# Performance work log

Measured on AMD Instinct MI355X. Metric: run time of the kernel, lower is better.

## Reference

```python
import jax, jax.numpy as jnp
import numpy as np
import math

IN_DIM = 512
OUT_DIM = 512
K = 64
N_BANDS = 3
TOTAL_K = K * N_BANDS
SCALE = 0.1
XAVIER_SCALE = math.sqrt(2.0 / (IN_DIM + OUT_DIM))


def setup_inputs() -> dict:
    key = jax.random.key(0)
    k_x, k_om, k_phi, k_a, k_ab = jax.random.split(key, 5)
    x = jax.random.normal(k_x, (8, 1024, IN_DIM), dtype=jnp.float32)
    # omega: per-band frequency scaling 1 + 3*band
    band_scales = jnp.repeat(1.0 + 3.0 * jnp.arange(N_BANDS, dtype=jnp.float32), K)  # (TOTAL_K,)
    omega = jax.random.normal(k_om, (TOTAL_K, 3), dtype=jnp.float32) * band_scales[:, None]
    phi = jax.random.normal(k_phi, (TOTAL_K,), dtype=jnp.float32) * math.pi
    n_coeff = 2 * TOTAL_K
    decay = 1.0 + jnp.arange(n_coeff, dtype=jnp.float32)
    alpha = jax.random.normal(k_a, (n_coeff,), dtype=jnp.float32) * 0.01 / decay
    alpha_bias = jax.random.normal(k_ab, (n_coeff,), dtype=jnp.float32) * 0.001
    return {"x": x, "omega": omega, "phi": phi, "alpha": alpha,
            "alpha_bias": alpha_bias, "layer_idx": 2, "num_layers": 6}


def _positions(layer_idx, num_layers):
    l_val = (layer_idx + 1.0) / (num_layers + 1.0)
    i_idx = (jnp.arange(IN_DIM, dtype=jnp.float32) + 1.0) / (IN_DIM + 1.0)
    j_idx = (jnp.arange(OUT_DIM, dtype=jnp.float32) + 1.0) / (OUT_DIM + 1.0)
    ii, jj = jnp.meshgrid(i_idx, j_idx, indexing='ij')
    ll = jnp.full_like(ii, l_val)
    pw = jnp.stack([ii, jj, ll], axis=-1).reshape(-1, 3)  # (IN*OUT, 3)
    pb = jnp.stack([jnp.zeros_like(j_idx), j_idx, jnp.full_like(j_idx, l_val)], axis=-1)  # (OUT, 3)
    return pw, pb


def reference(x, omega, phi, alpha, alpha_bias, layer_idx, num_layers):
    pw, pb = _positions(float(layer_idx), float(num_layers))
    # weight synthesis: tiny-K matmul -> sin/cos features -> reduce with alpha
    args = pw @ omega.T + phi                       # (IN*OUT, TOTAL_K)
    features = jnp.concatenate([jnp.sin(args), jnp.cos(args)], axis=1)  # (IN*OUT, 2K)
    W = (features @ alpha * SCALE).reshape(IN_DIM, OUT_DIM) * (XAVIER_SCALE / SCALE)
    # bias synthesis
    bargs = pb @ omega.T + phi                      # (OUT, TOTAL_K)
    bfeat = jnp.concatenate([jnp.sin(bargs), jnp.cos(bargs)], axis=1)
    b = bfeat @ alpha_bias * SCALE * 0.2            # (OUT,)
    return x @ W + b
```

## Files before the change

### kernel.cpp

```cpp
#include <hip/hip_runtime.h>
#include <hip/hip_bf16.h>
#include <math.h>

#define IN_DIM   512
#define OUT_DIM  512
#define NK       192
#define KF       384
#define XAVIER   0.04419417382415922f
#define BIAS_SCALE 0.02f

typedef __attribute__((ext_vector_type(8))) short bf16x8;
typedef __attribute__((ext_vector_type(4))) float f32x4;
typedef unsigned short u16;
typedef unsigned int   u32;
typedef unsigned long long u64;

__device__ inline u16 f2bf(float f) {
    __hip_bfloat16 h = __float2bfloat16(f);
    return *reinterpret_cast<u16*>(&h);
}
__device__ inline u32 pack2bf(float lo, float hi) {
    return (u32)f2bf(lo) | ((u32)f2bf(hi) << 16);
}
__device__ inline void gload_lds16(const void* g, void* l) {
    __builtin_amdgcn_global_load_lds(
        (const __attribute__((address_space(1))) void*)g,
        (__attribute__((address_space(3))) void*)l, 16, 0, 0);
}
__device__ inline void fsincos(float x, float& s, float& c) {
    float t = x * 0.15915494309189535f;
    t -= floorf(t);
    s = __builtin_amdgcn_sinf(t);
    c = __builtin_amdgcn_cosf(t);
}

__global__ __launch_bounds__(512) void synth_fused(
    const float* __restrict__ omega, const float* __restrict__ phi,
    const float* __restrict__ alpha, const float* __restrict__ alpha_bias,
    const int* __restrict__ layer_idx, const int* __restrict__ num_layers,
    u16* __restrict__ Wt, float* __restrict__ bias)
{
    const int b   = blockIdx.x;
    const int tid = threadIdx.x;
    const float l = ((float)layer_idx[0] + 1.0f) / ((float)num_layers[0] + 1.0f);

    __shared__ u16 sV[32 * KF];
    __shared__ u16 sU[32 * KF];
    __shared__ float bsc[4];

    const int bi = b & 15, bj = b >> 4;
    const int i0 = bi * 32, j0 = bj * 32;

    #pragma unroll 4
    for (int q = 0; q < 12; ++q) {
        const int e  = q * 512 + tid;
        const int rl = e / NK;
        const int k  = e - rl * NK;
        const int swz  = (rl & 7) << 4;
        const int base = rl * (KF * 2);
        const float om0 = omega[3*k], om1 = omega[3*k+1], om2 = omega[3*k+2];
        const float ph  = phi[k];
        {
            const float ii = (i0 + rl + 1.0f) * (1.0f / (IN_DIM + 1.0f));
            float s, c; fsincos(fmaf(ii, om0, fmaf(l, om2, ph)), s, c);
            *(u16*)((char*)sU + base + (((2*k)      ) ^ swz)) = f2bf(s);
            *(u16*)((char*)sU + base + (((2*k) + 384) ^ swz)) = f2bf(c);
        }
        {
            const float jj = (j0 + rl + 1.0f) * (1.0f / (OUT_DIM + 1.0f));
            float sv, cv; fsincos(jj * om1, sv, cv);
            const float as = alpha[k], ac = alpha[NK + k];
            *(u16*)((char*)sV + base + (((2*k)      ) ^ swz)) = f2bf((as*cv - ac*sv) * XAVIER);
            *(u16*)((char*)sV + base + (((2*k) + 384) ^ swz)) = f2bf((ac*cv + as*sv) * XAVIER);
        }
    }

    if (tid >= 256) {
        const int t2 = tid - 256;
        const int g  = t2 >> 7;
        const int k0 = t2 & 127;
        const int j  = 2*b + g;
        const float jj = (j + 1.0f) * (1.0f / (OUT_DIM + 1.0f));
        float bp = 0.0f;
        {
            float s, c;
            fsincos(fmaf(jj, omega[3*k0+1], fmaf(l, omega[3*k0+2], phi[k0])), s, c);
            bp = fmaf(alpha_bias[k0], s, fmaf(alpha_bias[NK + k0], c, bp));
        }
        if (k0 < 64) {
            const int k = k0 + 128;
            float s, c;
            fsincos(fmaf(jj, omega[3*k+1], fmaf(l, omega[3*k+2], phi[k])), s, c);
            bp = fmaf(alpha_bias[k], s, fmaf(alpha_bias[NK + k], c, bp));
        }
        #pragma unroll
        for (int off = 32; off > 0; off >>= 1)
            bp += __shfl_down(bp, off);
        if ((tid & 63) == 0) bsc[t2 >> 6] = bp;
    }
    __syncthreads();

    if (tid < 256) {
        const int wave = tid >> 6, lane = tid & 63;
        const int wr = wave >> 1, wc = wave & 1;
        f32x4 acc = {};
        #pragma unroll
        for (int kk = 0; kk < KF / 32; ++kk) {
            const int kb = kk * 64 + (lane >> 4) * 16;
            const int ra = wr*16 + (lane & 15);
            const int rb = wc*16 + (lane & 15);
            bf16x8 a = *reinterpret_cast<const bf16x8*>(
                (const char*)sV + ra*768 + (kb ^ ((ra & 7) << 4)));
            bf16x8 bb = *reinterpret_cast<const bf16x8*>(
                (const char*)sU + rb*768 + (kb ^ ((rb & 7) << 4)));
            acc = __builtin_amdgcn_mfma_f32_16x16x32_bf16(a, bb, acc, 0, 0, 0);
        }
        const int row = j0 + wr*16 + (lane >> 4) * 4;
        const int col = i0 + wc*16 + (lane & 15);
        #pragma unroll
        for (int r = 0; r < 4; ++r)
            Wt[(size_t)(row + r) * IN_DIM + col] = f2bf(acc[r]);
    }
    if (tid == 256) bias[2*b    ] = (bsc[0] + bsc[1]) * BIAS_SCALE;
    if (tid == 257) bias[2*b + 1] = (bsc[2] + bsc[3]) * BIAS_SCALE;
}

__global__ __launch_bounds__(512) void main_gemm(
    const float* __restrict__ X, const u16* __restrict__ Wt,
    const float* __restrict__ bias, float* __restrict__ out, int M)
{
    __shared__ u16 sA[2][32 * 64];
    __shared__ u16 sB[2][512 * 64];

    const int tid  = threadIdx.x;
    const int w    = tid >> 6, lane = tid & 63;
    const int brow = blockIdx.x * 32;

    f32x4 acc[2][4] = {};

    const int bsrc  = ((lane & 7) * 16) ^ ((lane >> 3) << 4);
    const int bjrow = lane >> 3;
    const int arow = tid >> 4;
    const int akq  = tid & 15;
    const int adst = arow * 128 + (((akq * 8)) ^ ((arow & 7) << 4));
    const size_t xoff = (size_t)(brow + arow) * IN_DIM + akq * 4;

    auto stageB = [&](int buf, int k0) {
        #pragma unroll
        for (int c = 0; c < 8; ++c) {
            const int ci = w * 8 + c;
            const int j  = ci * 8 + bjrow;
            gload_lds16((const char*)Wt + (size_t)j * (IN_DIM * 2) + k0 * 2 + bsrc,
                        (char*)&sB[buf][0] + ci * 1024);
        }
    };
    auto loadA = [&](int k0) -> f32x4 {
        return *reinterpret_cast<const f32x4*>(&X[xoff + k0]);
    };
    auto writeA = [&](int buf, f32x4 v) {
        u64 p = (u64)pack2bf(v.x, v.y) | ((u64)pack2bf(v.z, v.w) << 32);
        *reinterpret_cast<u64*>((char*)&sA[buf][0] + adst) = p;
    };
    auto compute = [&](int buf) {
        #pragma unroll
        for (int kk = 0; kk < 2; ++kk) {
            const int kb = kk * 64 + (lane >> 4) * 16;
            bf16x8 a[2], bb[4];
            #pragma unroll
            for (int m = 0; m < 2; ++m) {
                const int r = m*16 + (lane & 15);
                a[m] = *reinterpret_cast<const bf16x8*>(
                    (const char*)&sA[buf][0] + r*128 + (kb ^ ((r & 7) << 4)));
            }
            #pragma unroll
            for (int n = 0; n < 4; ++n) {
                const int j = w*64 + n*16 + (lane & 15);
                bb[n] = *reinterpret_cast<const bf16x8*>(
                    (const char*)&sB[buf][0] + j*128 + (kb ^ ((j & 7) << 4)));
            }
            #pragma unroll
            for (int m = 0; m < 2; ++m)
                #pragma unroll
                for (int n = 0; n < 4; ++n)
                    acc[m][n] = __builtin_amdgcn_mfma_f32_16x16x32_bf16(
                        a[m], bb[n], acc[m][n], 0, 0, 0);
        }
    };

    #define VMW(n)  asm volatile("s_waitcnt vmcnt(" #n ")" ::: "memory")
    #define LGKM0   asm volatile("s_waitcnt lgkmcnt(0)" ::: "memory")
    #define BARRIER do { __builtin_amdgcn_s_barrier(); \
                         asm volatile("" ::: "memory"); } while (0)

    {
        f32x4 av = loadA(0);
        stageB(0, 0);
        VMW(8);
        writeA(0, av);
        av = loadA(64);
        stageB(1, 64);
        VMW(8);
        writeA(1, av);
        LGKM0;
        BARRIER;
    }

    #pragma unroll
    for (int t = 0; t < 8; ++t) {
        compute(t & 1);
        BARRIER;
        if (t < 6) {
            f32x4 av = loadA((t + 2) * 64);
            stageB(t & 1, (t + 2) * 64);
            VMW(8);
            writeA(t & 1, av);
        } else if (t == 6) {
            VMW(0);
        }
        LGKM0;
        BARRIER;
    }

    #undef VMW
    #undef LGKM0
    #undef BARRIER

    #pragma unroll
    for (int n = 0; n < 4; ++n) {
        const int col = w*64 + n*16 + (lane & 15);
        const float bv = bias[col];
        #pragma unroll
        for (int m = 0; m < 2; ++m) {
            const int row0 = brow + m*16 + (lane >> 4) * 4;
            #pragma unroll
            for (int r = 0; r < 4; ++r)
                out[(size_t)(row0 + r) * OUT_DIM + col] = acc[m][n][r] + bv;
        }
    }
}

extern "C" void kernel_launch(void* const* d_in, const int* in_sizes, int n_in,
                              void* d_out, int out_size, void* d_ws, size_t ws_size,
                              hipStream_t stream) {
    const float* x          = (const float*)d_in[0];
    const float* omega      = (const float*)d_in[1];
    const float* phi        = (const float*)d_in[2];
    const float* alpha      = (const float*)d_in[3];
    const float* alpha_bias = (const float*)d_in[4];
    const int*   layer_idx  = (const int*)d_in[5];
    const int*   num_layers = (const int*)d_in[6];
    float* out = (float*)d_out;

    const int M = in_sizes[0] / IN_DIM;

    u16*   Wt   = (u16*)d_ws;
    float* bias = (float*)((char*)d_ws + 512 * 1024);

    synth_fused<<<256, 512, 0, stream>>>(omega, phi, alpha, alpha_bias,
                                         layer_idx, num_layers, Wt, bias);
    main_gemm<<<M / 32, 512, 0, stream>>>(x, Wt, bias, out, M);
}
```

Baseline: 24.14 us.

## Fuse weight synthesis and main GEMM into one kernel with grid barrier

Merges the synthesis kernel and the GEMM kernel into a single launch of M/32=256 blocks. Each block first synthesizes its weight tile and bias slice, then prefetches its first two X slices and waits on a global atomic counter until every block has finished, after which it runs the GEMM. The aim is to remove the second kernel launch and the gap between kernels, and to overlap the X loads with synthesis. In exchange it adds a memset launch and a spin-wait grid barrier. That barrier is only safe while all 256 blocks are co-resident, which the 136KB of shared memory per block makes dependent on CU count and occupancy.

Result: slower. 41.38 us (+71.4%).

```diff
diff --git a/kernel.cpp b/kernel.cpp
--- a/kernel.cpp
+++ b/kernel.cpp
@@ -34,110 +34,105 @@
     c = __builtin_amdgcn_cosf(t);
 }
 
-__global__ __launch_bounds__(512) void synth_fused(
+__global__ __launch_bounds__(512) void fourier_fused(
+    const float* __restrict__ X,
     const float* __restrict__ omega, const float* __restrict__ phi,
     const float* __restrict__ alpha, const float* __restrict__ alpha_bias,
     const int* __restrict__ layer_idx, const int* __restrict__ num_layers,
-    u16* __restrict__ Wt, float* __restrict__ bias)
+    u16* __restrict__ Wt, float* __restrict__ bias,
+    u32* __restrict__ ctr, float* __restrict__ out, int M)
 {
+    __shared__ __align__(16) char smem[136 * 1024];
+    char* const sA  = smem;
+    char* const sB  = smem + 8 * 1024;
+    char*  const sU  = smem + 72 * 1024;
+    char*  const sV  = smem + 96 * 1024;
+    float* const bsc = (float*)(smem + 120 * 1024);
+
     const int b   = blockIdx.x;
     const int tid = threadIdx.x;
     const float l = ((float)layer_idx[0] + 1.0f) / ((float)num_layers[0] + 1.0f);
 
-    __shared__ u16 sV[32 * KF];
-    __shared__ u16 sU[32 * KF];
-    __shared__ float bsc[4];
-
-    const int bi = b & 15, bj = b >> 4;
-    const int i0 = bi * 32, j0 = bj * 32;
-
-    #pragma unroll 4
-    for (int q = 0; q < 12; ++q) {
-        const int e  = q * 512 + tid;
-        const int rl = e / NK;
-        const int k  = e - rl * NK;
-        const int swz  = (rl & 7) << 4;
-        const int base = rl * (KF * 2);
-        const float om0 = omega[3*k], om1 = omega[3*k+1], om2 = omega[3*k+2];
-        const float ph  = phi[k];
-        {
-            const float ii = (i0 + rl + 1.0f) * (1.0f / (IN_DIM + 1.0f));
-            float s, c; fsincos(fmaf(ii, om0, fmaf(l, om2, ph)), s, c);
-            *(u16*)((char*)sU + base + (((2*k)      ) ^ swz)) = f2bf(s);
-            *(u16*)((char*)sU + base + (((2*k) + 384) ^ swz)) = f2bf(c);
-        }
-        {
-            const float jj = (j0 + rl + 1.0f) * (1.0f / (OUT_DIM + 1.0f));
-            float sv, cv; fsincos(jj * om1, sv, cv);
-            const float as = alpha[k], ac = alpha[NK + k];
-            *(u16*)((char*)sV + base + (((2*k)      ) ^ swz)) = f2bf((as*cv - ac*sv) * XAVIER);
-            *(u16*)((char*)sV + base + (((2*k) + 384) ^ swz)) = f2bf((ac*cv + as*sv) * XAVIER);
-        }
-    }
-
-    if (tid >= 256) {
-        const int t2 = tid - 256;
-        const int g  = t2 >> 7;
-        const int k0 = t2 & 127;
-        const int j  = 2*b + g;
-        const float jj = (j + 1.0f) * (1.0f / (OUT_DIM + 1.0f));
-        float bp = 0.0f;
-        {
-            float s, c;
-            fsincos(fmaf(jj, omega[3*k0+1], fmaf(l, omega[3*k0+2], phi[k0])), s, c);
-            bp = fmaf(alpha_bias[k0], s, fmaf(alpha_bias[NK + k0], c, bp));
-        }
-        if (k0 < 64) {
-            const int k = k0 + 128;
-            float s, c;
-            fsincos(fmaf(jj, omega[3*k+1], fmaf(l, omega[3*k+2], phi[k])), s, c);
-            bp = fmaf(alpha_bias[k], s, fmaf(alpha_bias[NK + k], c, bp));
-        }
-        #pragma unroll
-        for (int off = 32; off > 0; off >>= 1)
-            bp += __shfl_down(bp, off);
-        if ((tid & 63) == 0) bsc[t2 >> 6] = bp;
-    }
-    __syncthreads();
-
-    if (tid < 256) {
-        const int wave = tid >> 6, lane = tid & 63;
-        const int wr = wave >> 1, wc = wave & 1;
-        f32x4 acc = {};
-        #pragma unroll
-        for (int kk = 0; kk < KF / 32; ++kk) {
-            const int kb = kk * 64 + (lane >> 4) * 16;
-            const int ra = wr*16 + (lane & 15);
-            const int rb = wc*16 + (lane & 15);
-            bf16x8 a = *reinterpret_cast<const bf16x8*>(
-                (const char*)sV + ra*768 + (kb ^ ((ra & 7) << 4)));
-            bf16x8 bb = *reinterpret_cast<const bf16x8*>(
-                (const char*)sU + rb*768 + (kb ^ ((rb & 7) << 4)));
-            acc = __builtin_amdgcn_mfma_f32_16x16x32_bf16(a, bb, acc, 0, 0, 0);
-        }
-        const int row = j0 + wr*16 + (lane >> 4) * 4;
-        const int col = i0 + wc*16 + (lane & 15);
-        #pragma unroll
-        for (int r = 0; r < 4; ++r)
-            Wt[(size_t)(row + r) * IN_DIM + col] = f2bf(acc[r]);
-    }
-    if (tid == 256) bias[2*b    ] = (bsc[0] + bsc[1]) * BIAS_SCALE;
-    if (tid == 257) bias[2*b + 1] = (bsc[2] + bsc[3]) * BIAS_SCALE;
-}
-
-__global__ __launch_bounds__(512) void main_gemm(
-    const float* __restrict__ X, const u16* __restrict__ Wt,
-    const float* __restrict__ bias, float* __restrict__ out, int M)
-{
-    __shared__ u16 sA[2][32 * 64];
-    __shared__ u16 sB[2][512 * 64];
-
-    const int tid  = threadIdx.x;
+    {
+        const int bi = b & 15, bj = b >> 4;
+        const int i0 = bi * 32, j0 = bj * 32;
+
+        #pragma unroll 4
+        for (int q = 0; q < 12; ++q) {
+            const int e  = q * 512 + tid;
+            const int rl = e / NK;
+            const int k  = e - rl * NK;
+            const int swz  = (rl & 7) << 4;
+            const int base = rl * (KF * 2);
+            const float om0 = omega[3*k], om1 = omega[3*k+1], om2 = omega[3*k+2];
+            const float ph  = phi[k];
+            {
+                const float ii = (i0 + rl + 1.0f) * (1.0f / (IN_DIM + 1.0f));
+                float s, c; fsincos(fmaf(ii, om0, fmaf(l, om2, ph)), s, c);
+                *(u16*)(sU + base + (((2*k)      ) ^ swz)) = f2bf(s);
+                *(u16*)(sU + base + (((2*k) + 384) ^ swz)) = f2bf(c);
+            }
+            {
+                const float jj = (j0 + rl + 1.0f) * (1.0f / (OUT_DIM + 1.0f));
+                float sv, cv; fsincos(jj * om1, sv, cv);
+                const float as = alpha[k], ac = alpha[NK + k];
+                *(u16*)(sV + base + (((2*k)      ) ^ swz)) = f2bf((as*cv - ac*sv) * XAVIER);
+                *(u16*)(sV + base + (((2*k) + 384) ^ swz)) = f2bf((ac*cv + as*sv) * XAVIER);
+            }
+        }
+
+        if (tid >= 256) {
+            const int t2 = tid - 256;
+            const int g  = t2 >> 7;
+            const int k0 = t2 & 127;
+            const int j  = 2*b + g;
+            const float jj = (j + 1.0f) * (1.0f / (OUT_DIM + 1.0f));
+            float bp = 0.0f;
+            {
+                float s, c;
+                fsincos(fmaf(jj, omega[3*k0+1], fmaf(l, omega[3*k0+2], phi[k0])), s, c);
+                bp = fmaf(alpha_bias[k0], s, fmaf(alpha_bias[NK + k0], c, bp));
+            }
+            if (k0 < 64) {
+                const int k = k0 + 128;
+                float s, c;
+                fsincos(fmaf(jj, omega[3*k+1], fmaf(l, omega[3*k+2], phi[k])), s, c);
+                bp = fmaf(alpha_bias[k], s, fmaf(alpha_bias[NK + k], c, bp));
+            }
+            #pragma unroll
+            for (int off = 32; off > 0; off >>= 1)
+                bp += __shfl_down(bp, off);
+            if ((tid & 63) == 0) bsc[t2 >> 6] = bp;
+        }
+        __syncthreads();
+
+        if (tid < 256) {
+            const int wave = tid >> 6, lane = tid & 63;
+            const int wr = wave >> 1, wc = wave & 1;
+            f32x4 acc = {};
+            #pragma unroll
+            for (int kk = 0; kk < KF / 32; ++kk) {
+                const int kb = kk * 64 + (lane >> 4) * 16;
+                const int ra = wr*16 + (lane & 15);
+                const int rb = wc*16 + (lane & 15);
+                bf16x8 a = *reinterpret_cast<const bf16x8*>(
+                    sV + ra*768 + (kb ^ ((ra & 7) << 4)));
+                bf16x8 bb = *reinterpret_cast<const bf16x8*>(
+                    sU + rb*768 + (kb ^ ((rb & 7) << 4)));
+                acc = __builtin_amdgcn_mfma_f32_16x16x32_bf16(a, bb, acc, 0, 0, 0);
+            }
+            const int row = j0 + wr*16 + (lane >> 4) * 4;
+            const int col = i0 + wc*16 + (lane & 15);
+            #pragma unroll
+            for (int r = 0; r < 4; ++r)
+                Wt[(size_t)(row + r) * IN_DIM + col] = f2bf(acc[r]);
+        }
+        if (tid == 256) bias[2*b    ] = (bsc[0] + bsc[1]) * BIAS_SCALE;
+        if (tid == 257) bias[2*b + 1] = (bsc[2] + bsc[3]) * BIAS_SCALE;
+    }
+
     const int w    = tid >> 6, lane = tid & 63;
-    const int brow = blockIdx.x * 32;
-
-    f32x4 acc[2][4] = {};
-
+    const int brow = b * 32;
     const int bsrc  = ((lane & 7) * 16) ^ ((lane >> 3) << 4);
     const int bjrow = lane >> 3;
     const int arow = tid >> 4;
@@ -145,13 +140,27 @@
     const int adst = arow * 128 + (((akq * 8)) ^ ((arow & 7) << 4));
     const size_t xoff = (size_t)(brow + arow) * IN_DIM + akq * 4;
 
+    f32x4 av0 = *reinterpret_cast<const f32x4*>(&X[xoff]);
+    f32x4 av1 = *reinterpret_cast<const f32x4*>(&X[xoff + 64]);
+
+    __syncthreads();
+    if (tid == 0) {
+        __hip_atomic_fetch_add(ctr, 1u, __ATOMIC_ACQ_REL, __HIP_MEMORY_SCOPE_AGENT);
+        while (__hip_atomic_load(ctr, __ATOMIC_ACQUIRE, __HIP_MEMORY_SCOPE_AGENT)
+               < (u32)gridDim.x)
+            __builtin_amdgcn_s_sleep(2);
+    }
+    __syncthreads();
+
+    f32x4 acc[2][4] = {};
+
     auto stageB = [&](int buf, int k0) {
         #pragma unroll
         for (int c = 0; c < 8; ++c) {
             const int ci = w * 8 + c;
             const int j  = ci * 8 + bjrow;
             gload_lds16((const char*)Wt + (size_t)j * (IN_DIM * 2) + k0 * 2 + bsrc,
-                        (char*)&sB[buf][0] + ci * 1024);
+                        sB + buf * 65536 + ci * 1024);
         }
     };
     auto loadA = [&](int k0) -> f32x4 {
@@ -159,7 +168,7 @@
     };
     auto writeA = [&](int buf, f32x4 v) {
         u64 p = (u64)pack2bf(v.x, v.y) | ((u64)pack2bf(v.z, v.w) << 32);
-        *reinterpret_cast<u64*>((char*)&sA[buf][0] + adst) = p;
+        *reinterpret_cast<u64*>(sA + buf * 4096 + adst) = p;
     };
     auto compute = [&](int buf) {
         #pragma unroll
@@ -170,13 +179,13 @@
             for (int m = 0; m < 2; ++m) {
                 const int r = m*16 + (lane & 15);
                 a[m] = *reinterpret_cast<const bf16x8*>(
-                    (const char*)&sA[buf][0] + r*128 + (kb ^ ((r & 7) << 4)));
+                    sA + buf * 4096 + r*128 + (kb ^ ((r & 7) << 4)));
             }
             #pragma unroll
             for (int n = 0; n < 4; ++n) {
                 const int j = w*64 + n*16 + (lane & 15);
                 bb[n] = *reinterpret_cast<const bf16x8*>(
-                    (const char*)&sB[buf][0] + j*128 + (kb ^ ((j & 7) << 4)));
+                    sB + buf * 65536 + j*128 + (kb ^ ((j & 7) << 4)));
             }
             #pragma unroll
             for (int m = 0; m < 2; ++m)
@@ -192,18 +201,13 @@
     #define BARRIER do { __builtin_amdgcn_s_barrier(); \
                          asm volatile("" ::: "memory"); } while (0)
 
-    {
-        f32x4 av = loadA(0);
-        stageB(0, 0);
-        VMW(8);
-        writeA(0, av);
-        av = loadA(64);
-        stageB(1, 64);
-        VMW(8);
-        writeA(1, av);
-        LGKM0;
-        BARRIER;
-    }
+    stageB(0, 0);
+    stageB(1, 64);
+    writeA(0, av0);
+    writeA(1, av1);
+    VMW(8);
+    LGKM0;
+    BARRIER;
 
     #pragma unroll
     for (int t = 0; t < 8; ++t) {
@@ -255,8 +259,10 @@
 
     u16*   Wt   = (u16*)d_ws;
     float* bias = (float*)((char*)d_ws + 512 * 1024);
-
-    synth_fused<<<256, 512, 0, stream>>>(omega, phi, alpha, alpha_bias,
-                                         layer_idx, num_layers, Wt, bias);
-    main_gemm<<<M / 32, 512, 0, stream>>>(x, Wt, bias, out, M);
-}
+    u32*   ctr  = (u32*)((char*)d_ws + 516 * 1024);
+
+    hipMemsetAsync(ctr, 0, 4, stream);
+    fourier_fused<<<M / 32, 512, 0, stream>>>(
+        x, omega, phi, alpha, alpha_bias, layer_idx, num_layers,
+        Wt, bias, ctr, out, M);
+}
```

## Load whole A tile into LDS once and read Wt fragments directly from global

Applied to the files above, without the earlier changes.

The main GEMM now converts the block's full 32x512 slice of X to bf16 in LDS in a single pass behind one barrier. It reads the Wt MFMA operands straight from global memory (L2) instead of double-buffering them through LDS with async global_load_lds. Each wave only ever used its own 64 rows of the staged Wt, so the LDS copy gave no cross-wave reuse. Dropping it also removes the per-stage barriers and cuts LDS use from about 136KB to 32KB, which allows more blocks per CU. The cost is that the B loads are now exposed global-memory latency inside the MFMA loop, with only partially coalesced 64B segments per row.

New measurement: 30.44 us. +26.1%, slower.

```diff
diff --git a/kernel.cpp b/kernel.cpp
--- a/kernel.cpp
+++ b/kernel.cpp
@@ -21,11 +21,6 @@
 }
 __device__ inline u32 pack2bf(float lo, float hi) {
     return (u32)f2bf(lo) | ((u32)f2bf(hi) << 16);
-}
-__device__ inline void gload_lds16(const void* g, void* l) {
-    __builtin_amdgcn_global_load_lds(
-        (const __attribute__((address_space(1))) void*)g,
-        (__attribute__((address_space(3))) void*)l, 16, 0, 0);
 }
 __device__ inline void fsincos(float x, float& s, float& c) {
     float t = x * 0.15915494309189535f;
@@ -129,54 +124,49 @@
     const float* __restrict__ X, const u16* __restrict__ Wt,
     const float* __restrict__ bias, float* __restrict__ out, int M)
 {
-    __shared__ u16 sA[2][32 * 64];
-    __shared__ u16 sB[2][512 * 64];
+    __shared__ u16 sA[32 * 512];
 
     const int tid  = threadIdx.x;
     const int w    = tid >> 6, lane = tid & 63;
     const int brow = blockIdx.x * 32;
 
+    {
+        const int row = tid >> 4;
+        const int q   = tid & 15;
+        const int swz = (row & 7) << 4;
+        const float* src = X + (size_t)(brow + row) * IN_DIM;
+        #pragma unroll
+        for (int i = 0; i < 8; ++i) {
+            f32x4 v = *reinterpret_cast<const f32x4*>(src + q * 4 + i * 64);
+            const int byte = q * 8 + i * 128;
+            const int dst  = row * 1024 + (((byte & ~15) ^ swz) | (byte & 8));
+            u64 p = (u64)pack2bf(v.x, v.y) | ((u64)pack2bf(v.z, v.w) << 32);
+            *reinterpret_cast<u64*>((char*)sA + dst) = p;
+        }
+    }
+    __syncthreads();
+
+    const int lh = lane >> 4;
+    const int ll = lane & 15;
     f32x4 acc[2][4] = {};
 
-    const int bsrc  = ((lane & 7) * 16) ^ ((lane >> 3) << 4);
-    const int bjrow = lane >> 3;
-    const int arow = tid >> 4;
-    const int akq  = tid & 15;
-    const int adst = arow * 128 + (((akq * 8)) ^ ((arow & 7) << 4));
-    const size_t xoff = (size_t)(brow + arow) * IN_DIM + akq * 4;
-
-    auto stageB = [&](int buf, int k0) {
-        #pragma unroll
-        for (int c = 0; c < 8; ++c) {
-            const int ci = w * 8 + c;
-            const int j  = ci * 8 + bjrow;
-            gload_lds16((const char*)Wt + (size_t)j * (IN_DIM * 2) + k0 * 2 + bsrc,
-                        (char*)&sB[buf][0] + ci * 1024);
-        }
-    };
-    auto loadA = [&](int k0) -> f32x4 {
-        return *reinterpret_cast<const f32x4*>(&X[xoff + k0]);
-    };
-    auto writeA = [&](int buf, f32x4 v) {
-        u64 p = (u64)pack2bf(v.x, v.y) | ((u64)pack2bf(v.z, v.w) << 32);
-        *reinterpret_cast<u64*>((char*)&sA[buf][0] + adst) = p;
-    };
-    auto compute = [&](int buf) {
+    #pragma unroll
+    for (int s = 0; s < 8; ++s) {
         #pragma unroll
         for (int kk = 0; kk < 2; ++kk) {
-            const int kb = kk * 64 + (lane >> 4) * 16;
+            const int kel = s * 64 + kk * 32 + lh * 8;
             bf16x8 a[2], bb[4];
             #pragma unroll
             for (int m = 0; m < 2; ++m) {
-                const int r = m*16 + (lane & 15);
+                const int r = m * 16 + ll;
                 a[m] = *reinterpret_cast<const bf16x8*>(
-                    (const char*)&sA[buf][0] + r*128 + (kb ^ ((r & 7) << 4)));
+                    (const char*)sA + r * 1024 + ((kel * 2) ^ ((r & 7) << 4)));
             }
             #pragma unroll
             for (int n = 0; n < 4; ++n) {
-                const int j = w*64 + n*16 + (lane & 15);
+                const int j = w * 64 + n * 16 + ll;
                 bb[n] = *reinterpret_cast<const bf16x8*>(
-                    (const char*)&sB[buf][0] + j*128 + (kb ^ ((j & 7) << 4)));
+                    Wt + (size_t)j * IN_DIM + kel);
             }
             #pragma unroll
             for (int m = 0; m < 2; ++m)
@@ -185,53 +175,15 @@
                     acc[m][n] = __builtin_amdgcn_mfma_f32_16x16x32_bf16(
                         a[m], bb[n], acc[m][n], 0, 0, 0);
         }
-    };
-
-    #define VMW(n)  asm volatile("s_waitcnt vmcnt(" #n ")" ::: "memory")
-    #define LGKM0   asm volatile("s_waitcnt lgkmcnt(0)" ::: "memory")
-    #define BARRIER do { __builtin_amdgcn_s_barrier(); \
-                         asm volatile("" ::: "memory"); } while (0)
-
-    {
-        f32x4 av = loadA(0);
-        stageB(0, 0);
-        VMW(8);
-        writeA(0, av);
-        av = loadA(64);
-        stageB(1, 64);
-        VMW(8);
-        writeA(1, av);
-        LGKM0;
-        BARRIER;
-    }
-
-    #pragma unroll
-    for (int t = 0; t < 8; ++t) {
-        compute(t & 1);
-        BARRIER;
-        if (t < 6) {
-            f32x4 av = loadA((t + 2) * 64);
-            stageB(t & 1, (t + 2) * 64);
-            VMW(8);
-            writeA(t & 1, av);
-        } else if (t == 6) {
-            VMW(0);
-        }
-        LGKM0;
-        BARRIER;
-    }
-
-    #undef VMW
-    #undef LGKM0
-    #undef BARRIER
+    }
 
     #pragma unroll
     for (int n = 0; n < 4; ++n) {
-        const int col = w*64 + n*16 + (lane & 15);
+        const int col = w * 64 + n * 16 + ll;
         const float bv = bias[col];
         #pragma unroll
         for (int m = 0; m < 2; ++m) {
-            const int row0 = brow + m*16 + (lane >> 4) * 4;
+            const int row0 = brow + m * 16 + lh * 4;
             #pragma unroll
             for (int r = 0; r < 4; ++r)
                 out[(size_t)(row0 + r) * OUT_DIM + col] = acc[m][n][r] + bv;
```
